# Kernel tuning notes

Hardware: AMD Instinct MI355X
Metric: run time of the kernel (lower is better)

The kernel has to match this reference:

```python
import jax, jax.numpy as jnp
import numpy as np

N, DIM, H, HD = 2048, 1280, 16, 80

def _rotate_half(x):
    x1, x2 = x[..., :x.shape[-1] // 2], x[..., x.shape[-1] // 2:]
    return jnp.concatenate((-x2, x1), axis=-1)

def setup_inputs() -> dict:
    key = jax.random.key(0)
    ks = jax.random.split(key, 6)
    hidden_states = jax.random.normal(ks[0], (N, DIM), dtype=jnp.float32)
    cu_seqlens = jnp.array([0, N // 2, N], dtype=jnp.int32)  # 2 packed segments
    # rotary embeddings: half-dim inverse frequencies, duplicated to head_dim
    inv_freq = 1.0 / (10000.0 ** (np.arange(0, HD // 2, dtype=np.float32) * 2.0 / HD))
    pos = np.arange(N, dtype=np.float32) % (N // 2)  # positions restart per segment
    freqs = pos[:, None] * inv_freq[None, :]           # [N, HD/2]
    emb = jnp.asarray(np.concatenate([freqs, freqs], axis=-1))  # [N, HD]
    cos, sin = jnp.cos(emb), jnp.sin(emb)
    Wqkv = jax.random.normal(ks[1], (DIM, 3 * DIM), dtype=jnp.float32) * (DIM ** -0.5)
    bqkv = jax.random.normal(ks[2], (3 * DIM,), dtype=jnp.float32) * 0.02
    Wproj = jax.random.normal(ks[3], (DIM, DIM), dtype=jnp.float32) * (DIM ** -0.5)
    bproj = jax.random.normal(ks[4], (DIM,), dtype=jnp.float32) * 0.02
    return {"hidden_states": hidden_states, "cu_seqlens": cu_seqlens,
            "cos": cos, "sin": sin, "Wqkv": Wqkv, "bqkv": bqkv,
            "Wproj": Wproj, "bproj": bproj}

def reference(hidden_states, cu_seqlens, cos, sin, Wqkv, bqkv, Wproj, bproj):
    n = hidden_states.shape[0]
    scale = HD ** -0.5
    qkv = (hidden_states @ Wqkv + bqkv).reshape(n, 3, H, HD)
    q, k, v = qkv[:, 0], qkv[:, 1], qkv[:, 2]           # each [N, H, HD]
    # RoPE (fp32), cos/sin broadcast over heads: [N, 1, HD]
    c, s = cos[:, None, :], sin[:, None, :]
    q = q * c + _rotate_half(q) * s
    k = k * c + _rotate_half(k) * s
    # block-diagonal varlen mask from cu_seqlens (per-segment full attention)
    seg_id = jnp.searchsorted(cu_seqlens, jnp.arange(n), side='right')  # [N]
    mask = seg_id[:, None] == seg_id[None, :]                           # [N, N]
    scores = jnp.einsum('qhd,khd->hqk', q, k) * scale                   # [H, N, N]
    scores = jnp.where(mask[None], scores, -jnp.inf)
    attn = jax.nn.softmax(scores.astype(jnp.float32), axis=-1).astype(q.dtype)
    out = jnp.einsum('hqk,khd->qhd', attn, v).reshape(n, H * HD)        # [N, DIM]
    return out @ Wproj + bproj
```

## Files before the change

### kernel.cpp

```cpp
#include <hip/hip_runtime.h>
#include <hip/hip_bf16.h>

constexpr int N_TOK  = 2048;
constexpr int DIM    = 1280;
constexpr int NHEAD  = 16;
constexpr int HD     = 80;
constexpr int QKV_N  = 3 * DIM;

using bf16 = __hip_bfloat16;
typedef __attribute__((ext_vector_type(4)))  float f32x4;
typedef __attribute__((ext_vector_type(16))) float f32x16;
typedef __attribute__((ext_vector_type(8)))  short short8;
typedef unsigned int uint;

__device__ __forceinline__ float b2f(bf16 x) { return __bfloat162float(x); }
__device__ __forceinline__ bf16  f2b(float x) { return __float2bfloat16(x); }

__device__ __forceinline__ uint pk2(float a, float b) {
  __align__(4) bf16 t[2] = {f2b(a), f2b(b)};
  return *reinterpret_cast<uint*>(t);
}

typedef const __attribute__((address_space(1))) unsigned int* gas_u32;
typedef __attribute__((address_space(3))) unsigned int* las_u32;
__device__ __forceinline__ void gload_lds16(const void* g, void* l) {
  __builtin_amdgcn_global_load_lds((gas_u32)g, (las_u32)l, 16, 0, 0);
}

__device__ __forceinline__ void transpose_body(const float* __restrict__ W,
                                               bf16* __restrict__ WT, int K, int N) {
  __shared__ float tile[32][33];
  const int n0 = blockIdx.x * 32, k0 = blockIdx.y * 32;
  const int tc = threadIdx.x & 31, tr = threadIdx.x >> 5;
#pragma unroll
  for (int r = tr; r < 32; r += 8)
    tile[r][tc] = W[(size_t)(k0 + r) * N + n0 + tc];
  __syncthreads();
#pragma unroll
  for (int r = tr; r < 32; r += 8)
    WT[(size_t)(n0 + r) * K + k0 + tc] = f2b(tile[tc][r]);
}

__global__ __launch_bounds__(256)
void prep_kernel(const float* __restrict__ hs, bf16* __restrict__ hsb,
                 const float* __restrict__ Wqkv, bf16* __restrict__ WqkvT,
                 const float* __restrict__ Wproj, bf16* __restrict__ WprojT) {
  if (blockIdx.z == 0) {
    const int bid = blockIdx.y * gridDim.x + blockIdx.x;
    if (bid >= (N_TOK * DIM) / 2048) return;
    const int i = bid * 2048 + threadIdx.x * 8;
    const float4 a = *reinterpret_cast<const float4*>(hs + i);
    const float4 b = *reinterpret_cast<const float4*>(hs + i + 4);
    __align__(16) bf16 w[8] = {f2b(a.x), f2b(a.y), f2b(a.z), f2b(a.w),
                               f2b(b.x), f2b(b.y), f2b(b.z), f2b(b.w)};
    *reinterpret_cast<short8*>(hsb + i) = *reinterpret_cast<const short8*>(w);
  } else if (blockIdx.z == 1) {
    transpose_body(Wqkv, WqkvT, DIM, QKV_N);
  } else {
    if (blockIdx.x >= DIM / 32) return;
    transpose_body(Wproj, WprojT, DIM, DIM);
  }
}

template <int OBF>
__global__ __launch_bounds__(256)
void mfma_gemm(const bf16* __restrict__ A, const bf16* __restrict__ BT,
               const float* __restrict__ bias, void* __restrict__ C,
               int M, int N, int K) {
  __shared__ bf16 As[128 * 64];
  __shared__ bf16 Bs[128 * 64];
  const int tid = threadIdx.x;
  const int wid = tid >> 6, lane = tid & 63;
  const int lm = lane & 15, kg = lane >> 4;
  const int wm = (wid >> 1) * 64, wn = (wid & 1) * 64;
  const int m0 = blockIdx.y * 128, n0 = blockIdx.x * 128;

  const int srow = lane >> 3;
  const int sblk = (lane & 7) ^ srow;

  f32x4 acc[4][4];
#pragma unroll
  for (int i = 0; i < 4; ++i)
#pragma unroll
    for (int j = 0; j < 4; ++j) acc[i][j] = (f32x4){0.f, 0.f, 0.f, 0.f};

  for (int k0 = 0; k0 < K; k0 += 64) {
#pragma unroll
    for (int i = 0; i < 4; ++i) {
      const int slot = i * 4 + wid;
      const int row = slot * 8 + srow;
      gload_lds16(A + (size_t)(m0 + row) * K + k0 + sblk * 8, &As[slot * 512]);
      gload_lds16(BT + (size_t)(n0 + row) * K + k0 + sblk * 8, &Bs[slot * 512]);
    }
    __syncthreads();

#pragma unroll
    for (int kh = 0; kh < 2; ++kh) {
      short8 af[4], bfr[4];
#pragma unroll
      for (int t = 0; t < 4; ++t) {
        const int ar = wm + t * 16 + lm;
        af[t] = *reinterpret_cast<const short8*>(
            &As[ar * 64 + ((kh * 4 + kg) ^ (ar & 7)) * 8]);
        const int br = wn + t * 16 + lm;
        bfr[t] = *reinterpret_cast<const short8*>(
            &Bs[br * 64 + ((kh * 4 + kg) ^ (br & 7)) * 8]);
      }
#pragma unroll
      for (int mi = 0; mi < 4; ++mi)
#pragma unroll
        for (int ni = 0; ni < 4; ++ni)
          acc[mi][ni] = __builtin_amdgcn_mfma_f32_16x16x32_bf16(
              af[mi], bfr[ni], acc[mi][ni], 0, 0, 0);
    }
    __syncthreads();
  }

#pragma unroll
  for (int mi = 0; mi < 4; ++mi) {
#pragma unroll
    for (int ni = 0; ni < 4; ++ni) {
      const int col = n0 + wn + ni * 16 + lm;
      const float bv = bias[col];
#pragma unroll
      for (int r = 0; r < 4; ++r) {
        const int row = m0 + wm + mi * 16 + kg * 4 + r;
        const float v = acc[mi][ni][r] + bv;
        if constexpr (OBF)
          ((bf16*)C)[(size_t)row * N + col] = f2b(v);
        else
          ((float*)C)[(size_t)row * N + col] = v;
      }
    }
  }
}

__global__ __launch_bounds__(256)
void rope_k_kernel(bf16* __restrict__ qkv, const float* __restrict__ cosb,
                   const float* __restrict__ sinb) {
  const int idx = blockIdx.x * 256 + threadIdx.x;
  const int d0  = (idx % 5) * 8;
  const int h   = (idx / 5) % NHEAD;
  const int n   = idx / (5 * NHEAD);
  const size_t base = (size_t)n * QKV_N + DIM + h * HD;

  short8 a = *reinterpret_cast<const short8*>(qkv + base + d0);
  short8 b = *reinterpret_cast<const short8*>(qkv + base + 40 + d0);
  float cc1[8], cc2[8], ss1[8], ss2[8];
  *reinterpret_cast<float4*>(&cc1[0]) = *reinterpret_cast<const float4*>(cosb + n * HD + d0);
  *reinterpret_cast<float4*>(&cc1[4]) = *reinterpret_cast<const float4*>(cosb + n * HD + d0 + 4);
  *reinterpret_cast<float4*>(&cc2[0]) = *reinterpret_cast<const float4*>(cosb + n * HD + 40 + d0);
  *reinterpret_cast<float4*>(&cc2[4]) = *reinterpret_cast<const float4*>(cosb + n * HD + 44 + d0);
  *reinterpret_cast<float4*>(&ss1[0]) = *reinterpret_cast<const float4*>(sinb + n * HD + d0);
  *reinterpret_cast<float4*>(&ss1[4]) = *reinterpret_cast<const float4*>(sinb + n * HD + d0 + 4);
  *reinterpret_cast<float4*>(&ss2[0]) = *reinterpret_cast<const float4*>(sinb + n * HD + 40 + d0);
  *reinterpret_cast<float4*>(&ss2[4]) = *reinterpret_cast<const float4*>(sinb + n * HD + 44 + d0);

  __align__(16) bf16 o1[8], o2[8];
#pragma unroll
  for (int e = 0; e < 8; ++e) {
    const float x1 = b2f(reinterpret_cast<const bf16*>(&a)[e]);
    const float x2 = b2f(reinterpret_cast<const bf16*>(&b)[e]);
    o1[e] = f2b(x1 * cc1[e] - x2 * ss1[e]);
    o2[e] = f2b(x2 * cc2[e] + x1 * ss2[e]);
  }
  *reinterpret_cast<short8*>(qkv + base + d0)      = *reinterpret_cast<const short8*>(o1);
  *reinterpret_cast<short8*>(qkv + base + 40 + d0) = *reinterpret_cast<const short8*>(o2);
}

constexpr int KC   = 64;
constexpr int KSTR = 104;
constexpr int VSTR = 88;
constexpr int VROWS = 96;

__global__ __launch_bounds__(256)
void attn_mfma_kernel(const bf16* __restrict__ qkv, const int* __restrict__ cu,
                      const float* __restrict__ cosb, const float* __restrict__ sinb,
                      bf16* __restrict__ out, int nseg) {
  __shared__ bf16 Ks[2][KC * KSTR];
  __shared__ bf16 Vt[2][VROWS * VSTR];

  const int p = blockIdx.x;
  const int lidx = (p & 7) * (gridDim.x >> 3) + (p >> 3);
  const int xt  = lidx & 15;
  const int seg = (lidx >> 4) % nseg;
  const int h   = (lidx >> 4) / nseg;

  const int s0 = cu[seg], s1 = cu[seg + 1];
  if (s0 + xt * 128 >= s1) return;

  const int tid  = threadIdx.x;
  const int wid  = tid >> 6, lane = tid & 63;
  const int l31  = lane & 31;
  const int half = lane >> 5;
  const float scale = 0.11180339887498949f;

  const int qrow = s0 + xt * 128 + wid * 32 + l31;

#pragma unroll
  for (int t = 0; t < 2; ++t) {
    const int s = tid + t * 256;
    if (s < 352) {
      const int b = s / 176, rem = s % 176;
      const int r = 80 + rem / 11, sl = rem % 11;
      *reinterpret_cast<short8*>(&Vt[b][r * VSTR + sl * 8]) =
          (short8){0, 0, 0, 0, 0, 0, 0, 0};
    }
  }

  short8 qraw[5];
  const int nclamp = min(qrow, s1 - 1);
#pragma unroll
  for (int j = 0; j < 5; ++j) {
    const int dbase = j * 16 + half * 8;
    qraw[j] = (qrow < s1)
        ? *reinterpret_cast<const short8*>(qkv + (size_t)qrow * QKV_N + h * HD + dbase)
        : (short8){0, 0, 0, 0, 0, 0, 0, 0};
  }
  short8 part[5];
#pragma unroll
  for (int w = 0; w < 4; ++w) {
    const uint d0 = reinterpret_cast<const uint*>(&qraw[0])[w];
    const uint d1 = reinterpret_cast<const uint*>(&qraw[1])[w];
    const uint d2 = reinterpret_cast<const uint*>(&qraw[2])[w];
    const uint d3 = reinterpret_cast<const uint*>(&qraw[3])[w];
    const uint d4 = reinterpret_cast<const uint*>(&qraw[4])[w];
    auto s1p = __builtin_amdgcn_permlane32_swap(d2, d0, false, false);
    auto s2p = __builtin_amdgcn_permlane32_swap(d4, d2, false, false);
    auto s3p = __builtin_amdgcn_permlane32_swap(d0, d3, false, false);
    auto s4p = __builtin_amdgcn_permlane32_swap(d3, d1, false, false);
    auto s5p = __builtin_amdgcn_permlane32_swap(d1, d4, false, false);
    reinterpret_cast<uint*>(&part[0])[w] = half ? s3p[0] : s1p[1];
    reinterpret_cast<uint*>(&part[1])[w] = half ? s5p[0] : s4p[1];
    reinterpret_cast<uint*>(&part[2])[w] = half ? s1p[0] : s2p[1];
    reinterpret_cast<uint*>(&part[3])[w] = half ? s4p[0] : s3p[1];
    reinterpret_cast<uint*>(&part[4])[w] = half ? s2p[0] : s5p[1];
  }
  short8 qa[5];
  {
    const float* cq = cosb + nclamp * HD;
    const float* sq = sinb + nclamp * HD;
#pragma unroll
    for (int j = 0; j < 5; ++j) {
      const int dbase = j * 16 + half * 8;
      float cv[8], sv[8];
      *reinterpret_cast<float4*>(&cv[0]) = *reinterpret_cast<const float4*>(cq + dbase);
      *reinterpret_cast<float4*>(&cv[4]) = *reinterpret_cast<const float4*>(cq + dbase + 4);
      *reinterpret_cast<float4*>(&sv[0]) = *reinterpret_cast<const float4*>(sq + dbase);
      *reinterpret_cast<float4*>(&sv[4]) = *reinterpret_cast<const float4*>(sq + dbase + 4);
      const float sgn = (dbase < 40) ? -1.f : 1.f;
      __align__(16) bf16 o[8];
#pragma unroll
      for (int e = 0; e < 8; ++e) {
        const float x  = b2f(reinterpret_cast<const bf16*>(&qraw[j])[e]);
        const float xp = b2f(reinterpret_cast<const bf16*>(&part[j])[e]);
        o[e] = f2b(x * cv[e] + sgn * xp * sv[e]);
      }
      qa[j] = *reinterpret_cast<const short8*>(o);
    }
  }

  short8 kreg[3], vreg[4];
  const int vgrp = tid / 10, vsl = tid % 10;
  auto issueK = [&](int c) {
    const int k0 = s0 + c * KC;
#pragma unroll
    for (int t = 0; t < 3; ++t) {
      const int s = tid + t * 256;
      if (s < 640) {
        const int r = min(k0 + s / 10, s1 - 1);
        kreg[t] = *reinterpret_cast<const short8*>(
            qkv + (size_t)r * QKV_N + DIM + h * HD + (s % 10) * 8);
      }
    }
  };
  auto commitK = [&](int buf) {
#pragma unroll
    for (int t = 0; t < 3; ++t) {
      const int s = tid + t * 256;
      if (s < 640)
        *reinterpret_cast<short8*>(&Ks[buf][(s / 10) * KSTR + (s % 10) * 8]) =
            kreg[t];
    }
  };
  auto issueV = [&](int c) {
    if (tid < 160) {
      const int k0 = s0 + c * KC;
#pragma unroll
      for (int e = 0; e < 4; ++e) {
        const int r = min(k0 + vgrp * 4 + e, s1 - 1);
        vreg[e] = *reinterpret_cast<const short8*>(
            qkv + (size_t)r * QKV_N + 2 * DIM + h * HD + vsl * 8);
      }
    }
  };
  auto commitV = [&](int buf) {
    if (tid < 160) {
      const int r0 = vgrp * 4;
      const int swz = (vsl & 7) << 3;
#pragma unroll
      for (int de = 0; de < 8; ++de) {
        __align__(8) bf16 w[4] = {reinterpret_cast<const bf16*>(&vreg[0])[de],
                                  reinterpret_cast<const bf16*>(&vreg[1])[de],
                                  reinterpret_cast<const bf16*>(&vreg[2])[de],
                                  reinterpret_cast<const bf16*>(&vreg[3])[de]};
        *reinterpret_cast<uint2*>(&Vt[buf][(vsl * 8 + de) * VSTR + (r0 ^ swz)]) =
            *reinterpret_cast<const uint2*>(w);
      }
    }
  };

  f32x16 oacc[3];
#pragma unroll
  for (int dt = 0; dt < 3; ++dt)
#pragma unroll
    for (int r = 0; r < 16; ++r) oacc[dt][r] = 0.f;
  float m = -1e30f, l = 0.f;
  const int nch = (s1 - s0 + KC - 1) / KC;

  issueK(0);
  issueV(0);
  commitK(0);
  commitV(0);
  if (nch > 1) {
    issueK(1);
    issueV(1);
  }
  __syncthreads();

  for (int c = 0; c < nch; ++c) {
    const int cur = c & 1;
    const int nk = min(KC, s1 - (s0 + c * KC));

    f32x16 sc[2];
    __builtin_amdgcn_s_setprio(1);
#pragma unroll
    for (int kt = 0; kt < 2; ++kt) {
#pragma unroll
      for (int r = 0; r < 16; ++r) sc[kt][r] = 0.f;
#pragma unroll
      for (int ck = 0; ck < 5; ++ck) {
        short8 ka = *reinterpret_cast<const short8*>(
            &Ks[cur][(kt * 32 + l31) * KSTR + ck * 16 + half * 8]);
        sc[kt] = __builtin_amdgcn_mfma_f32_32x32x16_bf16(ka, qa[ck], sc[kt], 0, 0, 0);
      }
    }
    __builtin_amdgcn_s_setprio(0);

    if (c + 1 < nch) {
      commitK(cur ^ 1);
      commitV(cur ^ 1);
    }
    if (c + 2 < nch) {
      issueK(c + 2);
      issueV(c + 2);
    }

#pragma unroll
    for (int kt = 0; kt < 2; ++kt)
#pragma unroll
      for (int r = 0; r < 16; ++r) sc[kt][r] *= scale;
    if (nk < KC) {
#pragma unroll
      for (int kt = 0; kt < 2; ++kt)
#pragma unroll
        for (int r = 0; r < 16; ++r) {
          const int key = kt * 32 + (r & 3) + 8 * (r >> 2) + 4 * half;
          if (key >= nk) sc[kt][r] = -1e30f;
        }
    }
    float rml = sc[0][0];
#pragma unroll
    for (int kt = 0; kt < 2; ++kt)
#pragma unroll
      for (int r = 0; r < 16; ++r)
        if (kt | r) rml = fmaxf(rml, sc[kt][r]);
    if (!__all(rml - m <= 8.0f)) {
      float rm = fmaxf(rml, __shfl_xor(rml, 32));
      const float mnew = fmaxf(m, rm);
      const float fs = __expf(m - mnew);
      m = mnew;
      l *= fs;
#pragma unroll
      for (int dt = 0; dt < 3; ++dt)
#pragma unroll
        for (int r = 0; r < 16; ++r) oacc[dt][r] *= fs;
    }
#pragma unroll
    for (int kt = 0; kt < 2; ++kt)
#pragma unroll
      for (int r = 0; r < 16; ++r) {
        sc[kt][r] = __expf(sc[kt][r] - m);
        l += sc[kt][r];
      }

    uint pbw[4][4];
#pragma unroll
    for (int kt = 0; kt < 2; ++kt) {
      uint w[8];
#pragma unroll
      for (int i = 0; i < 8; ++i) w[i] = pk2(sc[kt][2 * i], sc[kt][2 * i + 1]);
#pragma unroll
      for (int kc2 = 0; kc2 < 2; ++kc2) {
        auto r02 = __builtin_amdgcn_permlane32_swap(w[4 * kc2 + 0],
                                                    w[4 * kc2 + 2], false, false);
        auto r13 = __builtin_amdgcn_permlane32_swap(w[4 * kc2 + 1],
                                                    w[4 * kc2 + 3], false, false);
        pbw[kt * 2 + kc2][0] = r02[0];
        pbw[kt * 2 + kc2][1] = r13[0];
        pbw[kt * 2 + kc2][2] = r02[1];
        pbw[kt * 2 + kc2][3] = r13[1];
      }
    }

    __builtin_amdgcn_s_setprio(1);
#pragma unroll
    for (int kc = 0; kc < 4; ++kc) {
      short8 pb = *reinterpret_cast<const short8*>(&pbw[kc][0]);
#pragma unroll
      for (int dt = 0; dt < 3; ++dt) {
        const int d = dt * 32 + l31;
        short8 va = *reinterpret_cast<const short8*>(
            &Vt[cur][d * VSTR + ((kc * 16 + half * 8) ^ (((d >> 3) & 7) << 3))]);
        oacc[dt] = __builtin_amdgcn_mfma_f32_32x32x16_bf16(va, pb, oacc[dt], 0, 0, 0);
      }
    }
    __builtin_amdgcn_s_setprio(0);

    __syncthreads();
  }

  l += __shfl_xor(l, 32);
  if (qrow < s1) {
    const float inv = 1.f / l;
    bf16* op = out + (size_t)qrow * DIM + h * HD;
#pragma unroll
    for (int dt = 0; dt < 3; ++dt) {
#pragma unroll
      for (int g = 0; g < 4; ++g) {
        const int d = dt * 32 + g * 8 + half * 4;
        if (d < HD) {
          __align__(8) bf16 w[4] = {f2b(oacc[dt][g * 4 + 0] * inv),
                                    f2b(oacc[dt][g * 4 + 1] * inv),
                                    f2b(oacc[dt][g * 4 + 2] * inv),
                                    f2b(oacc[dt][g * 4 + 3] * inv)};
          *reinterpret_cast<uint2*>(op + d) = *reinterpret_cast<const uint2*>(w);
        }
      }
    }
  }
}

extern "C" void kernel_launch(void* const* d_in, const int* in_sizes, int n_in,
                              void* d_out, int out_size, void* d_ws, size_t ws_size,
                              hipStream_t stream) {
  const float* hs    = (const float*)d_in[0];
  const int*   cu    = (const int*)d_in[1];
  const float* cosb  = (const float*)d_in[2];
  const float* sinb  = (const float*)d_in[3];
  const float* Wqkv  = (const float*)d_in[4];
  const float* bqkv  = (const float*)d_in[5];
  const float* Wproj = (const float*)d_in[6];
  const float* bproj = (const float*)d_in[7];

  bf16* qkv      = (bf16*)d_ws;
  bf16* attn_out = qkv + (size_t)N_TOK * QKV_N;
  bf16* WqkvT    = attn_out + (size_t)N_TOK * DIM;
  bf16* WprojT   = WqkvT + (size_t)QKV_N * DIM;
  bf16* hsb      = WprojT + (size_t)DIM * DIM;

  prep_kernel<<<dim3(QKV_N / 32, DIM / 32, 3), 256, 0, stream>>>(
      hs, hsb, Wqkv, WqkvT, Wproj, WprojT);

  mfma_gemm<1><<<dim3(QKV_N / 128, N_TOK / 128), 256, 0, stream>>>(
      hsb, WqkvT, bqkv, qkv, N_TOK, QKV_N, DIM);

  rope_k_kernel<<<(N_TOK * NHEAD * 5) / 256, 256, 0, stream>>>(qkv, cosb, sinb);

  int nseg = in_sizes[1] - 1;
  int nblk = (N_TOK / 128) * nseg * NHEAD;
  attn_mfma_kernel<<<nblk, 256, 0, stream>>>(qkv, cu, cosb, sinb, attn_out, nseg);

  mfma_gemm<0><<<dim3(DIM / 128, N_TOK / 128), 256, 0, stream>>>(
      attn_out, WprojT, bproj, d_out, N_TOK, DIM, DIM);
}
```

Before: 111.9 us.

## Load K tiles directly into LDS and remap GEMM block order

K chunks in the attention kernel are now loaded with direct global-to-LDS loads into an unpadded layout (stride 80), replacing register staging and the separate commit step. The K prefetch distance shrinks from two chunks to one, issued right after the score MFMAs. The GEMM also remaps block indices in an 8-way interleave to improve L2 locality. The unpadded K stride risks LDS bank conflicts on MFMA operand reads, and the shorter prefetch may expose more global load latency.

```diff
diff --git a/kernel.cpp b/kernel.cpp
--- a/kernel.cpp
+++ b/kernel.cpp
@@ -73,7 +73,11 @@
   const int wid = tid >> 6, lane = tid & 63;
   const int lm = lane & 15, kg = lane >> 4;
   const int wm = (wid >> 1) * 64, wn = (wid & 1) * 64;
-  const int m0 = blockIdx.y * 128, n0 = blockIdx.x * 128;
+
+  const int nblk = gridDim.x * gridDim.y;
+  const int bid  = blockIdx.y * gridDim.x + blockIdx.x;
+  const int lbid = (bid & 7) * (nblk >> 3) + (bid >> 3);
+  const int m0 = (lbid / gridDim.x) * 128, n0 = (lbid % gridDim.x) * 128;
 
   const int srow = lane >> 3;
   const int sblk = (lane & 7) ^ srow;
@@ -169,7 +173,7 @@
 }
 
 constexpr int KC   = 64;
-constexpr int KSTR = 104;
+constexpr int KSTR = 80;
 constexpr int VSTR = 88;
 constexpr int VROWS = 96;
 
@@ -260,29 +264,22 @@
     }
   }
 
-  short8 kreg[3], vreg[4];
+  auto gloadK = [&](int c, int buf) {
+    const int k0 = s0 + c * KC;
+#pragma unroll
+    for (int i = 0; i < 3; ++i) {
+      const int si = wid + i * 4;
+      if (si < 10) {
+        const int elem = si * 512 + lane * 8;
+        const int r = elem / 80, cc = elem % 80;
+        const int row = min(k0 + r, s1 - 1);
+        gload_lds16(qkv + (size_t)row * QKV_N + DIM + h * HD + cc,
+                    &Ks[buf][si * 512]);
+      }
+    }
+  };
+  short8 vreg[4];
   const int vgrp = tid / 10, vsl = tid % 10;
-  auto issueK = [&](int c) {
-    const int k0 = s0 + c * KC;
-#pragma unroll
-    for (int t = 0; t < 3; ++t) {
-      const int s = tid + t * 256;
-      if (s < 640) {
-        const int r = min(k0 + s / 10, s1 - 1);
-        kreg[t] = *reinterpret_cast<const short8*>(
-            qkv + (size_t)r * QKV_N + DIM + h * HD + (s % 10) * 8);
-      }
-    }
-  };
-  auto commitK = [&](int buf) {
-#pragma unroll
-    for (int t = 0; t < 3; ++t) {
-      const int s = tid + t * 256;
-      if (s < 640)
-        *reinterpret_cast<short8*>(&Ks[buf][(s / 10) * KSTR + (s % 10) * 8]) =
-            kreg[t];
-    }
-  };
   auto issueV = [&](int c) {
     if (tid < 160) {
       const int k0 = s0 + c * KC;
@@ -318,14 +315,10 @@
   float m = -1e30f, l = 0.f;
   const int nch = (s1 - s0 + KC - 1) / KC;
 
-  issueK(0);
+  gloadK(0, 0);
   issueV(0);
-  commitK(0);
   commitV(0);
-  if (nch > 1) {
-    issueK(1);
-    issueV(1);
-  }
+  if (nch > 1) issueV(1);
   __syncthreads();
 
   for (int c = 0; c < nch; ++c) {
@@ -348,13 +341,10 @@
     __builtin_amdgcn_s_setprio(0);
 
     if (c + 1 < nch) {
-      commitK(cur ^ 1);
+      gloadK(c + 1, cur ^ 1);
       commitV(cur ^ 1);
     }
-    if (c + 2 < nch) {
-      issueK(c + 2);
-      issueV(c + 2);
-    }
+    if (c + 2 < nch) issueV(c + 2);
 
 #pragma unroll
     for (int kt = 0; kt < 2; ++kt)
```

Result: no change. 112.8 us (+0.8%).
